# Performance work log

Hardware: AMD Instinct MI355X
Metric: run time of the kernel (lower is better)

## Reference

```python
import jax, jax.numpy as jnp
import numpy as np

HEADS = 8; KVH = 4; HD = 64; MULT = 2; DIFF = 1; DIM = 512; K = 3
LAMBDA_INIT = 0.2          # 0.8 - 0.6*exp(-0.3*layer_idx), layer_idx=0, affine=False
EPS = 1e-8
ROPE_CONST = 10000.0


def conv2d(x, w):
    # SAME padding (=1) for k=3, stride 1, zeros padding mode, no bias
    return jax.lax.conv_general_dilated(x, w, (1, 1), [(1, 1), (1, 1)],
                                        dimension_numbers=('NCHW', 'OIHW', 'NCHW'))


def rope(x):
    # x: [B, S, h, D]; rotate interleaved pairs (torch view_as_complex layout)
    D = x.shape[-1]; S = x.shape[1]
    theta = 1.0 / (ROPE_CONST ** (jnp.arange(0, D, 2, dtype=jnp.float32) / D))
    ang = jnp.arange(S, dtype=jnp.float32)[:, None] * theta[None, :]      # [S, D/2]
    cos = jnp.cos(ang)[None, :, None, :]
    sin = jnp.sin(ang)[None, :, None, :]
    xr = x.reshape(*x.shape[:-1], D // 2, 2)
    x0, x1 = xr[..., 0], xr[..., 1]
    out = jnp.stack([x0 * cos - x1 * sin, x0 * sin + x1 * cos], axis=-1)
    return out.reshape(x.shape)


def setup_inputs() -> dict:
    key = jax.random.key(0)
    ks = jax.random.split(key, 10)
    conv_std = 1.0 / np.sqrt(DIM * K * K)
    x = jax.random.normal(ks[0], (1, 2, DIM, 64, 64), jnp.float32)
    cross = jax.random.normal(ks[1], (1, 2, DIM, 32, 32), jnp.float32)
    wq = jax.random.normal(ks[2], (HEADS * HD * MULT, DIM, K, K), jnp.float32) * conv_std
    wk = jax.random.normal(ks[3], (KVH * HD * MULT, DIM, K, K), jnp.float32) * conv_std
    wv = jax.random.normal(ks[4], (KVH * HD, DIM, K, K), jnp.float32) * conv_std
    wo = jax.random.normal(ks[5], (DIM, DIM, K, K), jnp.float32) * conv_std
    # lambda params scaled to keep exp(sum over head_dim) numerically sane
    lam_q1 = jax.random.normal(ks[6], (HEADS, HD, DIFF), jnp.float32) * 0.05
    lam_q2 = jax.random.normal(ks[7], (HEADS, HD, DIFF), jnp.float32) * 0.05
    lam_k1 = jax.random.normal(ks[8], (HEADS, HD, DIFF), jnp.float32) * 0.05
    lam_k2 = jax.random.normal(ks[9], (HEADS, HD, DIFF), jnp.float32) * 0.05
    return {'x': x, 'cross': cross, 'wq': wq, 'wk': wk, 'wv': wv, 'wo': wo,
            'lam_q1': lam_q1, 'lam_q2': lam_q2, 'lam_k1': lam_k1, 'lam_k2': lam_k2}


def reference(x, cross, wq, wk, wv, wo, lam_q1, lam_q2, lam_k1, lam_k2):
    g, b, c, H, W = x.shape
    _, _, _, Hc, Wc = cross.shape
    B = g * b; Sq = H * W; Sk = Hc * Wc
    xb = x.reshape(B, c, H, W)
    cb = cross.reshape(B, c, Hc, Wc)
    # conv QKV projections
    q = conv2d(xb, wq)                     # [B, heads*HD*MULT, H, W]
    k = conv2d(cb, wk)                     # [B, KVH*HD*MULT, Hc, Wc]
    v = conv2d(cb, wv)                     # [B, KVH*HD, Hc, Wc]
    # convert: channels are head-major -> [B, S, heads, HD*mult]
    q = q.reshape(B, HEADS, HD * MULT, Sq).transpose(0, 3, 1, 2)
    k = k.reshape(B, KVH, HD * MULT, Sk).transpose(0, 3, 1, 2)
    v = v.reshape(B, KVH, HD, Sk).transpose(0, 3, 1, 2)
    # RoPE over flattened pixel positions, rotating full HD*MULT per head
    q = rope(q)
    k = rope(k)
    # grouped-query: repeat kv heads
    rep = HEADS // KVH
    k = jnp.repeat(k, rep, axis=2)         # [B, Sk, heads, HD*MULT]
    v = jnp.repeat(v, rep, axis=2)         # [B, Sk, heads, HD]
    # split into 1+DIFF score components
    qm = q.reshape(B, Sq, HEADS, MULT, HD)
    km = k.reshape(B, Sk, HEADS, MULT, HD)
    scale = 1.0 / np.sqrt(HD)
    scores = jnp.einsum('bqhmd,bkhmd->bhmqk', qm, km) * scale
    attn = jax.nn.softmax(scores, axis=-1)               # [B, h, MULT, Sq, Sk]
    # differential lambda: ((exp(sum q1*k1) - exp(sum q2*k2)) + init) * (-1)^i
    signs = (-1.0) ** jnp.arange(1, DIFF + 1, dtype=jnp.float32)   # [DIFF]
    lam = (jnp.exp(jnp.sum(lam_q1 * lam_k1, axis=-2))
           - jnp.exp(jnp.sum(lam_q2 * lam_k2, axis=-2)) + LAMBDA_INIT) * signs  # [h, DIFF]
    combined = attn[:, :, 0] + jnp.einsum('hm,bhmqk->bhqk', lam, attn[:, :, 1:])
    out = jnp.einsum('bhqk,bkhd->bqhd', combined, v)     # [B, Sq, h, HD]
    # per-head RMSNorm (affine=False) then post-attention shift
    out = out * jax.lax.rsqrt(jnp.mean(out * out, axis=-1, keepdims=True) + EPS)
    out = out * (1.0 - LAMBDA_INIT)
    # revert to image layout and output conv
    out = out.reshape(B, Sq, HEADS * HD).transpose(0, 2, 1).reshape(B, c, H, W)
    out = conv2d(out, wo)
    return out.reshape(g, b, c, H, W)
```

## Files before the change

kernel.cpp:

```cpp
#include <hip/hip_runtime.h>


typedef __attribute__((ext_vector_type(8))) short short8;
typedef __attribute__((ext_vector_type(4))) float f32x4;
typedef unsigned short us;

__device__ __forceinline__ float bf2f(us u) {
  union { unsigned int i; float f; } v; v.i = ((unsigned int)u) << 16; return v.f;
}
__device__ __forceinline__ us f2bf(float f) {
  union { float f; unsigned int i; } v; v.f = f;
  unsigned int x = v.i;
  return (us)((x + 0x7fffu + ((x >> 16) & 1u)) >> 16);
}

typedef __attribute__((address_space(3))) unsigned int as3_uint;
typedef const __attribute__((address_space(1))) unsigned int as1_uint;
__device__ __forceinline__ void gload16(const us* g, us* l) {
  __builtin_amdgcn_global_load_lds((as1_uint*)g, (as3_uint*)l, 16, 0, 0);
}
__device__ __forceinline__ unsigned int cvt_pk_bf16(float a, float b) {
  unsigned int r;
  asm("v_cvt_pk_bf16_f32 %0, %1, %2" : "=v"(r) : "v"(a), "v"(b));
  return r;
}
__device__ __forceinline__ float fast_exp2(float x) {
  float r;
  asm("v_exp_f32 %0, %1" : "=v"(r) : "v"(x));
  return r;
}

__device__ __forceinline__ void transpose_body(
    const float* __restrict__ in, us* __restrict__ outT,
    int b, int y, int ci0, int H, int W, int logW) {
  const int C = 512;
  int padW = W + 2, Ppad = (H + 2) * padW;
  __shared__ float tile[64][65];
  int nt = W * 64;
  for (int idx = threadIdx.x; idx < nt; idx += 256) {
    int ci = idx >> logW, x = idx & (W - 1);
    tile[ci][x] = in[(((size_t)b * C + ci0 + ci) * H + y) * W + x];
  }
  __syncthreads();
  int nt2 = W * 32;
  for (int idx = threadIdx.x; idx < nt2; idx += 256) {
    int px = idx >> 5, c2 = idx & 31;
    unsigned int val = (unsigned int)f2bf(tile[c2 * 2][px]) |
                       ((unsigned int)f2bf(tile[c2 * 2 + 1][px]) << 16);
    *(unsigned int*)(outT + ((size_t)b * Ppad + (size_t)(y + 1) * padW + (px + 1)) * C +
                     ci0 + c2 * 2) = val;
  }
}

__global__ __launch_bounds__(256) void prep_all(
    const float* __restrict__ x, const float* __restrict__ cross,
    const float* __restrict__ wq, const float* __restrict__ wk,
    const float* __restrict__ wv, const float* __restrict__ wo,
    const float* __restrict__ lq1, const float* __restrict__ lq2,
    const float* __restrict__ lk1, const float* __restrict__ lk2,
    us* __restrict__ xpadT, us* __restrict__ cpadT, us* __restrict__ apad,
    us* __restrict__ oq, us* __restrict__ ok, us* __restrict__ ov,
    us* __restrict__ oo, float* __restrict__ lam) {
  int bid = blockIdx.x, tid = threadIdx.x;
  if (bid < 326) {
    int g = bid * 4 + (tid >> 6);
    int t = tid & 63;
    us* base; int W, b, i;
    if (g < 520)      { base = xpadT; W = 64; b = g >= 260; i = g - b * 260; }
    else if (g < 784) { base = cpadT; W = 32; int gg = g - 520; b = gg >= 132; i = gg - b * 132; }
    else              { base = apad; W = 64; int gg = g - 784; b = gg >= 260; i = gg - b * 260; }
    int padW = W + 2, nb = 2 * padW;
    int yy, xx;
    if (i < padW)    { yy = 0; xx = i; }
    else if (i < nb) { yy = W + 1; xx = i - padW; }
    else             { int j = i - nb; yy = 1 + (j >> 1); xx = (j & 1) * (W + 1); }
    size_t p = ((size_t)b * padW * padW + (size_t)yy * padW + xx) * 512 + t * 8;
    *(int4*)(base + p) = make_int4(0, 0, 0, 0);
  } else if (bid < 1350) {
    int i = bid - 326;
    transpose_body(x, xpadT, i >> 9, (i >> 3) & 63, (i & 7) * 64, 64, 64, 6);
  } else if (bid < 1862) {
    int i = bid - 1350;
    transpose_body(cross, cpadT, i >> 8, (i >> 3) & 31, (i & 7) * 64, 32, 32, 5);
  } else if (bid < 4166) {
    int blk = bid - 1862;
    const float* src; us* dst; int Cout, co;
    if (blk < 1024)      { src = wq; dst = oq; Cout = 1024; co = blk; }
    else if (blk < 1536) { src = wk; dst = ok; Cout = 512;  co = blk - 1024; }
    else if (blk < 1792) { src = wv; dst = ov; Cout = 256;  co = blk - 1536; }
    else                 { src = wo; dst = oo; Cout = 512;  co = blk - 1792; }
    __shared__ us l[4608];
    const float* s0 = src + (size_t)co * 4608;
#pragma unroll
    for (int k = 0; k < 18; ++k) { int i = k * 256 + tid; l[i] = f2bf(s0[i]); }
    __syncthreads();
#pragma unroll
    for (int k = 0; k < 9; ++k) {
      int j = k * 256 + tid;
      int t = j >> 8, c2 = j & 255;
      unsigned int val = (unsigned int)l[(c2 * 2) * 9 + t] |
                         ((unsigned int)l[(c2 * 2 + 1) * 9 + t] << 16);
      *(unsigned int*)(dst + (size_t)t * Cout * 512 + (size_t)co * 512 + c2 * 2) = val;
    }
  } else {
    int h = tid >> 5, d = tid & 31;
    float s1 = lq1[h * 64 + d] * lk1[h * 64 + d] +
               lq1[h * 64 + d + 32] * lk1[h * 64 + d + 32];
    float s2 = lq2[h * 64 + d] * lk2[h * 64 + d] +
               lq2[h * 64 + d + 32] * lk2[h * 64 + d + 32];
    for (int m = 16; m; m >>= 1) {
      s1 += __shfl_xor(s1, m);
      s2 += __shfl_xor(s2, m);
    }
    if (d == 0) lam[h] = -(expf(s1) - expf(s2) + 0.2f);
  }
}

__device__ __forceinline__ void conv128_body(
    const us* __restrict__ inT, const us* __restrict__ wp,
    us* __restrict__ out, int Cout, int bid, us* sh) {
  int v = (bid & 7) * 64 + (bid >> 3);
  int pxt = v & 31, cot = (v >> 5) & 7, b = v >> 8;
  int p0 = pxt * 128, co0 = cot * 128;
  int tid = threadIdx.x;
  int wave = tid >> 6, lane = tid & 63, l15 = lane & 15, hi4 = lane >> 4;
  int wr = wave >> 1, wc = wave & 1;
  f32x4 acc[4][4];
#pragma unroll
  for (int m = 0; m < 4; ++m)
#pragma unroll
    for (int n = 0; n < 4; ++n) acc[m][n] = (f32x4){0.f, 0.f, 0.f, 0.f};

  int arow[4], brow[4];
#pragma unroll
  for (int c = 0; c < 4; ++c) {
    int row = c * 32 + (tid >> 3);
    int g = (tid & 7) ^ (row & 7);
    int px = p0 + row;
    int y = px >> 6, x = px & 63;
    arow[c] = (y * 66 + x) * 512 + g * 8;
    brow[c] = (co0 + row) * 512 + g * 8;
  }
  int aoff[4][2], boff[4][2];
#pragma unroll
  for (int m = 0; m < 4; ++m)
#pragma unroll
    for (int ks = 0; ks < 2; ++ks) {
      int ra = wr * 64 + m * 16 + l15;
      int rb = wc * 64 + m * 16 + l15;
      aoff[m][ks] = ra * 64 + (((ks * 4 + hi4) ^ (l15 & 7)) * 8);
      boff[m][ks] = rb * 64 + (((ks * 4 + hi4) ^ (l15 & 7)) * 8);
    }
  const us* abase = inT + (size_t)b * 66 * 66 * 512;

  auto stage = [&](int buf, int s) {
    int tn = s >> 3, ci = (s & 7) << 6;
    int ky = (tn * 11) >> 5, kx = tn - ky * 3;
    const us* as = abase + (ky * 66 + kx) * 512 + ci;
    const us* bs = wp + (size_t)tn * Cout * 512 + ci;
    us* la = sh + buf * 16384;
    us* lb = la + 8192;
#pragma unroll
    for (int c = 0; c < 4; ++c) {
      gload16(as + arow[c], la + c * 2048 + wave * 512);
      gload16(bs + brow[c], lb + c * 2048 + wave * 512);
    }
  };

  stage(0, 0);
  __syncthreads();
  for (int s = 0; s < 72; ++s) {
    int cur = s & 1;
    if (s < 71) stage(cur ^ 1, s + 1);
    const us* la = sh + cur * 16384;
    const us* lb = la + 8192;
#pragma unroll
    for (int ks = 0; ks < 2; ++ks) {
      short8 af[4], bf[4];
#pragma unroll
      for (int m = 0; m < 4; ++m) af[m] = *(const short8*)(la + aoff[m][ks]);
#pragma unroll
      for (int n = 0; n < 4; ++n) bf[n] = *(const short8*)(lb + boff[n][ks]);
#pragma unroll
      for (int m = 0; m < 4; ++m)
#pragma unroll
        for (int n = 0; n < 4; ++n)
          acc[m][n] = __builtin_amdgcn_mfma_f32_16x16x32_bf16(af[m], bf[n], acc[m][n], 0, 0, 0);
    }
    __syncthreads();
  }
  int par = lane & 1;
#pragma unroll
  for (int n = 0; n < 4; ++n) {
    int co = co0 + wc * 64 + n * 16 + l15;
    int j = (co & 127) >> 1;
    float th = exp2f(-(float)j * 0.20762050593f);
    float sth, cth;
    sincosf(th, &sth, &cth);
#pragma unroll
    for (int m = 0; m < 4; ++m) {
      int pxb = p0 + wr * 64 + m * 16 + hi4 * 4;
      float s0, c0;
      sincosf((float)pxb * th, &s0, &c0);
#pragma unroll
      for (int r = 0; r < 4; ++r) {
        float xv = acc[m][n][r];
        float ov = __shfl_xor(xv, 1);
        float y = par ? fmaf(ov, s0, xv * c0) : fmaf(xv, c0, -ov * s0);
        out[((size_t)b * 4096 + (pxb + r)) * Cout + co] = f2bf(y);
        float c1 = c0 * cth - s0 * sth;
        s0 = fmaf(c0, sth, s0 * cth);
        c0 = c1;
      }
    }
  }
}

template <int TRANS_OUT, int ROPE>
__device__ __forceinline__ void conv64_body(
    const us* __restrict__ inT, const us* __restrict__ wp,
    us* __restrict__ out, int Cout, int logCoT, int bid, int ngrid, us* sh) {
  int nchunk = ngrid >> 3;
  int v = (bid & 7) * nchunk + (bid >> 3);
  int yt = v & 15;
  int cot = (v >> 4) & ((1 << logCoT) - 1);
  int b = v >> (4 + logCoT);
  int p0 = yt * 64, co0 = cot * 64;
  const int W = 32, logW = 5, padW = 34, HW = 1024;
  int tid = threadIdx.x;
  int wave = tid >> 6, lane = tid & 63, l15 = lane & 15, hi4 = lane >> 4;
  f32x4 acc[4];
#pragma unroll
  for (int i = 0; i < 4; ++i) acc[i] = (f32x4){0.f, 0.f, 0.f, 0.f};

  int arow[2], brow[2];
#pragma unroll
  for (int c = 0; c < 2; ++c) {
    int row = (wave * 2 + c) * 8 + (lane >> 3);
    int g = (lane & 7) ^ (row & 7);
    int px = p0 + row;
    int y = px >> logW, x = px & (W - 1);
    arow[c] = (y * padW + x) * 512 + g * 8;
    brow[c] = (co0 + row) * 512 + g * 8;
  }
  int gb[2];
#pragma unroll
  for (int ks = 0; ks < 2; ++ks) gb[ks] = ((ks * 4 + hi4) ^ (l15 & 7)) * 8;

  const us* abase = inT + (size_t)b * padW * padW * 512;

  auto stage = [&](int buf, int s) {
    int tn = s >> 3, ci = (s & 7) << 6;
    int ky = (tn * 11) >> 5, kx = tn - ky * 3;
    const us* as = abase + (ky * padW + kx) * 512 + ci;
    const us* bs = wp + (size_t)tn * Cout * 512 + ci;
    us* la = sh + buf * 8192;
    us* lb = la + 4096;
#pragma unroll
    for (int c = 0; c < 2; ++c) {
      gload16(as + arow[c], la + (wave * 2 + c) * 512);
      gload16(bs + brow[c], lb + (wave * 2 + c) * 512);
    }
  };

  stage(0, 0);
  __syncthreads();
  for (int s = 0; s < 72; ++s) {
    int cur = s & 1;
    if (s < 71) stage(cur ^ 1, s + 1);
    const us* la = sh + cur * 8192;
    const us* lb = la + 4096;
#pragma unroll
    for (int ks = 0; ks < 2; ++ks) {
      short8 bf = *(const short8*)(lb + (16 * wave + l15) * 64 + gb[ks]);
#pragma unroll
      for (int i = 0; i < 4; ++i) {
        short8 af = *(const short8*)(la + (i * 16 + l15) * 64 + gb[ks]);
        acc[i] = __builtin_amdgcn_mfma_f32_16x16x32_bf16(af, bf, acc[i], 0, 0, 0);
      }
    }
    __syncthreads();
  }
  if (ROPE) {
    int co = co0 + 16 * wave + l15;
    int j = (co & 127) >> 1;
    float th = exp2f(-(float)j * 0.20762050593f);
    float sth, cth;
    sincosf(th, &sth, &cth);
    int par = lane & 1;
#pragma unroll
    for (int i = 0; i < 4; ++i) {
      int pxb = p0 + i * 16 + hi4 * 4;
      float s0, c0;
      sincosf((float)pxb * th, &s0, &c0);
#pragma unroll
      for (int r = 0; r < 4; ++r) {
        float xv = acc[i][r];
        float ov = __shfl_xor(xv, 1);
        float y = par ? fmaf(ov, s0, xv * c0) : fmaf(xv, c0, -ov * s0);
        out[((size_t)b * HW + (pxb + r)) * Cout + co] = f2bf(y);
        float c1 = c0 * cth - s0 * sth;
        s0 = fmaf(c0, sth, s0 * cth);
        c0 = c1;
      }
    }
  } else {
#pragma unroll
    for (int i = 0; i < 4; ++i)
#pragma unroll
      for (int r = 0; r < 4; ++r) {
        int px = TRANS_OUT ? (p0 + (hi4 * 4 + r) * 4 + i)
                           : (p0 + i * 16 + hi4 * 4 + r);
        int co = co0 + 16 * wave + l15;
        us val = f2bf(acc[i][r]);
        if (TRANS_OUT)
          out[((size_t)b * Cout + co) * HW + px] = val;
        else
          out[((size_t)b * HW + px) * Cout + co] = val;
      }
  }
}

__global__ __launch_bounds__(256) void conv_qkv(
    const us* __restrict__ xpadT, const us* __restrict__ cpadT,
    const us* __restrict__ wqp, const us* __restrict__ wkp,
    const us* __restrict__ wvp, us* __restrict__ qb,
    us* __restrict__ kb, us* __restrict__ vT) {
  __shared__ __align__(16) us sh[2][2][128][64];
  int bid = blockIdx.x;
  if (bid < 256)      conv64_body<0, 1>(cpadT, wkp, kb, 512, 3, bid, 256, &sh[0][0][0][0]);
  else if (bid < 384) conv64_body<1, 0>(cpadT, wvp, vT, 256, 2, bid - 256, 128, &sh[0][0][0][0]);
  else                conv128_body(xpadT, wqp, qb, 1024, bid - 384, &sh[0][0][0][0]);
}

__global__ __launch_bounds__(256) void conv128_out(
    const us* __restrict__ apad, const us* __restrict__ wp,
    float* __restrict__ out) {
  int bid = blockIdx.x;
  int v = (bid & 7) * 32 + (bid >> 3);
  int pxt = v & 31, cot = (v >> 5) & 3, b = v >> 7;
  int p0 = pxt * 128, co0 = cot * 128;
  int tid = threadIdx.x;
  int wave = tid >> 6, lane = tid & 63, l15 = lane & 15, hi4 = lane >> 4;
  int wr = wave >> 1, wc = wave & 1;
  __shared__ __align__(16) us lds[2][2][128][64];
  f32x4 acc[4][4];
#pragma unroll
  for (int m = 0; m < 4; ++m)
#pragma unroll
    for (int n = 0; n < 4; ++n) acc[m][n] = (f32x4){0.f, 0.f, 0.f, 0.f};

  int arow[4], brow[4];
#pragma unroll
  for (int c = 0; c < 4; ++c) {
    int row = c * 32 + (tid >> 3);
    int g = (tid & 7) ^ (row & 7);
    arow[c] = (co0 + row) * 512 + g * 8;
    int px = p0 + row;
    int y = px >> 6, x = px & 63;
    brow[c] = (y * 66 + x) * 512 + g * 8;
  }
  int aoff[4][2], boff[4][2];
#pragma unroll
  for (int m = 0; m < 4; ++m)
#pragma unroll
    for (int ks = 0; ks < 2; ++ks) {
      int ra = wr * 64 + m * 16 + l15;
      int rb = wc * 64 + m * 16 + l15;
      aoff[m][ks] = ra * 64 + (((ks * 4 + hi4) ^ (l15 & 7)) * 8);
      boff[m][ks] = rb * 64 + (((ks * 4 + hi4) ^ (l15 & 7)) * 8);
    }
  const us* bbase = apad + (size_t)b * 4356 * 512;

  auto stage = [&](int buf, int s) {
    int tn = s >> 3, ci = (s & 7) << 6;
    int ky = (tn * 11) >> 5, kx = tn - ky * 3;
    const us* as = wp + (size_t)tn * 512 * 512 + ci;
    const us* bs = bbase + (ky * 66 + kx) * 512 + ci;
    us* la = &lds[buf][0][0][0];
    us* lb = &lds[buf][1][0][0];
#pragma unroll
    for (int c = 0; c < 4; ++c) {
      gload16(as + arow[c], la + c * 2048 + wave * 512);
      gload16(bs + brow[c], lb + c * 2048 + wave * 512);
    }
  };

  stage(0, 0);
  __syncthreads();
  for (int s = 0; s < 72; ++s) {
    int cur = s & 1;
    if (s < 71) stage(cur ^ 1, s + 1);
    const us* la = &lds[cur][0][0][0];
    const us* lb = &lds[cur][1][0][0];
#pragma unroll
    for (int ks = 0; ks < 2; ++ks) {
      short8 af[4], bf[4];
#pragma unroll
      for (int m = 0; m < 4; ++m) af[m] = *(const short8*)(la + aoff[m][ks]);
#pragma unroll
      for (int n = 0; n < 4; ++n) bf[n] = *(const short8*)(lb + boff[n][ks]);
#pragma unroll
      for (int m = 0; m < 4; ++m)
#pragma unroll
        for (int n = 0; n < 4; ++n)
          acc[m][n] = __builtin_amdgcn_mfma_f32_16x16x32_bf16(af[m], bf[n], acc[m][n], 0, 0, 0);
    }
    __syncthreads();
  }
#pragma unroll
  for (int m = 0; m < 4; ++m)
#pragma unroll
    for (int n = 0; n < 4; ++n)
#pragma unroll
      for (int r = 0; r < 4; ++r) {
        int co = co0 + wr * 64 + m * 16 + hi4 * 4 + r;
        int px = p0 + wc * 64 + n * 16 + l15;
        out[((size_t)b * 512 + co) * 4096 + px] = acc[m][n][r];
      }
}

__global__ __launch_bounds__(256) void attn_kernel(
    const us* __restrict__ qb, const us* __restrict__ kb,
    const us* __restrict__ vT, const float* __restrict__ lam,
    us* __restrict__ apad) {
  int qt = blockIdx.x, h = blockIdx.y, b = blockIdx.z;
  int kvh = h >> 1;
  int tid = threadIdx.x;
  int wave = tid >> 6, lane = tid & 63, l15 = lane & 15, hi4 = lane >> 4;
  __shared__ __align__(16) us Klds[2][8192];
  __shared__ __align__(16) us Vlds[2][4096];
  __shared__ __align__(16) us Plds[4][16][72];

  int q0 = qt * 128;
  short8 qf[2][2][2];
  {
    const us* qsrc =
        qb + ((size_t)(b * 4096 + q0 + wave * 32 + l15)) * 1024 + h * 128 + hi4 * 8;
#pragma unroll
    for (int mf = 0; mf < 2; ++mf)
#pragma unroll
      for (int m = 0; m < 2; ++m)
#pragma unroll
        for (int ks = 0; ks < 2; ++ks)
          qf[mf][m][ks] = *(const short8*)(qsrc + mf * 16384 + m * 64 + ks * 32);
  }

  float sumd[2][2][4];
  f32x4 accO[2][2][4];
#pragma unroll
  for (int mf = 0; mf < 2; ++mf)
#pragma unroll
    for (int m = 0; m < 2; ++m)
#pragma unroll
      for (int r = 0; r < 4; ++r) {
        sumd[mf][m][r] = 0.f;
        accO[mf][m][r] = (f32x4){0.f, 0.f, 0.f, 0.f};
      }
  float lamh = lam[h];

  const us* kbase0 = kb + (size_t)b * 524288 + kvh * 128;
  const us* vbase0 = vT + ((size_t)(b * 256 + kvh * 64)) * 1024;
  int krow[4], vrow[2];
#pragma unroll
  for (int c = 0; c < 4; ++c) {
    int row = (wave * 4 + c) * 4 + hi4;
    int g = (l15 & 8) | ((l15 & 7) ^ (row & 7));
    krow[c] = row * 512 + g * 8;
  }
#pragma unroll
  for (int c = 0; c < 2; ++c) {
    int row = (wave * 2 + c) * 8 + (lane >> 3);
    int g = (lane & 7) ^ (row & 7);
    vrow[c] = row * 1024 + g * 8;
  }
  int kg0[2], kg1[2], vg[2];
#pragma unroll
  for (int m = 0; m < 2; ++m) {
    kg0[m] = (m * 8 | (hi4 ^ (l15 & 7))) * 8;
    kg1[m] = (m * 8 | ((4 + hi4) ^ (l15 & 7))) * 8;
  }
#pragma unroll
  for (int ks = 0; ks < 2; ++ks) vg[ks] = ((ks * 4 + hi4) ^ (l15 & 7)) * 8;

  auto stage = [&](int buf, int kt2) {
    const us* kk = kbase0 + (size_t)kt2 * 32768;
    const us* vv = vbase0 + kt2 * 64;
#pragma unroll
    for (int c = 0; c < 4; ++c)
      gload16(kk + krow[c], &Klds[buf][(wave * 4 + c) * 512]);
#pragma unroll
    for (int c = 0; c < 2; ++c)
      gload16(vv + vrow[c], &Vlds[buf][(wave * 2 + c) * 512]);
  };

  const float cexp = 0.18033688f;
  stage(0, 0);
  for (int kt = 0; kt < 16; ++kt) {
    int cur = kt & 1;
    if (kt < 15) {
      stage(cur ^ 1, kt + 1);
      asm volatile("s_waitcnt vmcnt(6)" ::: "memory");
    } else {
      asm volatile("s_waitcnt vmcnt(0)" ::: "memory");
    }
    __builtin_amdgcn_s_barrier();
    __builtin_amdgcn_sched_barrier(0);

    short8 vf[2][4];
#pragma unroll
    for (int ks = 0; ks < 2; ++ks)
#pragma unroll
      for (int nf = 0; nf < 4; ++nf)
        vf[ks][nf] = *(const short8*)&Vlds[cur][(nf * 16 + l15) * 64 + vg[ks]];

#pragma unroll
    for (int m = 0; m < 2; ++m) {
      short8 kf[4][2];
#pragma unroll
      for (int nf = 0; nf < 4; ++nf) {
        kf[nf][0] = *(const short8*)&Klds[cur][(nf * 16 + l15) * 128 + kg0[m]];
        kf[nf][1] = *(const short8*)&Klds[cur][(nf * 16 + l15) * 128 + kg1[m]];
      }
#pragma unroll
      for (int mf = 0; mf < 2; ++mf) {
        f32x4 s[4];
        __builtin_amdgcn_s_setprio(1);
#pragma unroll
        for (int nf = 0; nf < 4; ++nf) {
          f32x4 z = (f32x4){0.f, 0.f, 0.f, 0.f};
          z = __builtin_amdgcn_mfma_f32_16x16x32_bf16(qf[mf][m][0], kf[nf][0], z, 0, 0, 0);
          z = __builtin_amdgcn_mfma_f32_16x16x32_bf16(qf[mf][m][1], kf[nf][1], z, 0, 0, 0);
          s[nf] = z;
        }
        __builtin_amdgcn_s_setprio(0);
#pragma unroll
        for (int r = 0; r < 4; ++r) {
          float p0 = fast_exp2(s[0][r] * cexp);
          float p1 = fast_exp2(s[1][r] * cexp);
          float p2 = fast_exp2(s[2][r] * cexp);
          float p3 = fast_exp2(s[3][r] * cexp);
          sumd[mf][m][r] += (p0 + p1) + (p2 + p3);
          unsigned int w0 = cvt_pk_bf16(p0, p1);
          unsigned int w1 = cvt_pk_bf16(p2, p3);
          *(uint2*)&Plds[wave][hi4 * 4 + r][l15 * 4] = make_uint2(w0, w1);
        }
        __builtin_amdgcn_s_setprio(1);
#pragma unroll
        for (int ks = 0; ks < 2; ++ks) {
          short8 pf = *(const short8*)&Plds[wave][l15][ks * 32 + hi4 * 8];
#pragma unroll
          for (int nf = 0; nf < 4; ++nf)
            accO[mf][m][nf] =
                __builtin_amdgcn_mfma_f32_16x16x32_bf16(pf, vf[ks][nf], accO[mf][m][nf], 0, 0, 0);
        }
        __builtin_amdgcn_s_setprio(0);
      }
    }
    asm volatile("s_waitcnt lgkmcnt(0)" ::: "memory");
    __builtin_amdgcn_s_barrier();
    __builtin_amdgcn_sched_barrier(0);
  }

#pragma unroll
  for (int mf = 0; mf < 2; ++mf)
#pragma unroll
    for (int m = 0; m < 2; ++m)
#pragma unroll
      for (int r = 0; r < 4; ++r) {
        float sx = sumd[mf][m][r];
        sx += __shfl_xor(sx, 1);
        sx += __shfl_xor(sx, 2);
        sx += __shfl_xor(sx, 4);
        sx += __shfl_xor(sx, 8);
        sumd[mf][m][r] = sx;
      }
#pragma unroll
  for (int mf = 0; mf < 2; ++mf)
#pragma unroll
    for (int r = 0; r < 4; ++r) {
      float inv0 = 1.f / sumd[mf][0][r];
      float inv1 = lamh / sumd[mf][1][r];
      float comb[4];
      float ss = 0.f;
#pragma unroll
      for (int nf = 0; nf < 4; ++nf) {
        comb[nf] = accO[mf][0][nf][r] * inv0 + accO[mf][1][nf][r] * inv1;
        ss += comb[nf] * comb[nf];
      }
      ss += __shfl_xor(ss, 1);
      ss += __shfl_xor(ss, 2);
      ss += __shfl_xor(ss, 4);
      ss += __shfl_xor(ss, 8);
      float sc = rsqrtf(ss * (1.f / 64.f) + 1e-8f) * 0.8f;
      int q = q0 + wave * 32 + mf * 16 + hi4 * 4 + r;
      int y = q >> 6, x = q & 63;
      size_t oaddr = ((size_t)b * 4356 + (size_t)(y + 1) * 66 + (x + 1)) * 512 + h * 64;
#pragma unroll
      for (int nf = 0; nf < 4; ++nf) apad[oaddr + nf * 16 + l15] = f2bf(comb[nf] * sc);
    }
}

extern "C" void kernel_launch(void* const* d_in, const int* in_sizes, int n_in,
                              void* d_out, int out_size, void* d_ws, size_t ws_size,
                              hipStream_t stream) {
  const float* x     = (const float*)d_in[0];
  const float* cross = (const float*)d_in[1];
  const float* wq    = (const float*)d_in[2];
  const float* wk    = (const float*)d_in[3];
  const float* wv    = (const float*)d_in[4];
  const float* wo    = (const float*)d_in[5];
  const float* lq1   = (const float*)d_in[6];
  const float* lq2   = (const float*)d_in[7];
  const float* lk1   = (const float*)d_in[8];
  const float* lk2   = (const float*)d_in[9];
  float* out = (float*)d_out;

  char* ws = (char*)d_ws;
  size_t off = 0;
  auto nxt = [&](size_t bytes) { char* p = ws + off; off += bytes; return p; };
  us* xpadT = (us*)nxt(8921088);
  us* cpadT = (us*)nxt(2367488);
  us* apad  = (us*)nxt(8921088);
  us* wqp = (us*)nxt(9437184);
  us* wkp = (us*)nxt(4718592);
  us* wvp = (us*)nxt(2359296);
  us* wop = (us*)nxt(4718592);
  us* qb  = (us*)nxt(16777216);
  us* kb  = (us*)nxt(2097152);
  us* vT  = (us*)nxt(1048576);
  float* lam = (float*)nxt(256);
  (void)ws_size; (void)in_sizes; (void)n_in; (void)out_size;

  prep_all<<<4167, 256, 0, stream>>>(x, cross, wq, wk, wv, wo,
                                     lq1, lq2, lk1, lk2,
                                     xpadT, cpadT, apad, wqp, wkp, wvp, wop, lam);
  conv_qkv<<<896, 256, 0, stream>>>(xpadT, cpadT, wqp, wkp, wvp, qb, kb, vT);
  attn_kernel<<<dim3(32, 8, 2), 256, 0, stream>>>(qb, kb, vT, lam, apad);
  conv128_out<<<256, 256, 0, stream>>>(apad, wop, out);
}
```

Before: 261.2 us.

## Reuse padded input rows in LDS across 3x3 taps in Q and output convs

The Q projection conv and output conv are rewritten as one templated kernel. It stages a block of padded image rows (a halo) for a 32-channel slice into LDS once and reuses it for all nine filter taps, instead of reloading the shifted activation tile for every tap. Weights stream through a 4-deep ring buffer with explicit vmcnt waits and raw barriers. The K/V convs are split into their own launch, and the output conv now uses 128x64 tiles with twice as many blocks. This adds a kernel launch, uses finer-grained 32-channel K steps, and relies on hand-tuned wait counts whose correctness is fragile.

```diff
diff --git a/kernel.cpp b/kernel.cpp
--- a/kernel.cpp
+++ b/kernel.cpp
@@ -116,103 +116,152 @@
   }
 }
 
-__device__ __forceinline__ void conv128_body(
-    const us* __restrict__ inT, const us* __restrict__ wp,
-    us* __restrict__ out, int Cout, int bid, us* sh) {
+template <int MODE>
+__global__ __launch_bounds__(256) void conv_main(
+    const us* __restrict__ pix,
+    const us* __restrict__ wp,
+    us* __restrict__ outb, float* __restrict__ outf) {
+  constexpr int NR = (MODE == 0) ? 4 : 2;
+  constexpr int Cout = (MODE == 0) ? 1024 : 512;
+  constexpr int RROWS = (MODE == 0) ? 264 : 198;
+  constexpr int AROUNDS = (MODE == 0) ? 5 : 4;
+  int bid = blockIdx.x;
   int v = (bid & 7) * 64 + (bid >> 3);
-  int pxt = v & 31, cot = (v >> 5) & 7, b = v >> 8;
-  int p0 = pxt * 128, co0 = cot * 128;
+  int b, p0, co0;
+  if (MODE == 0) { p0 = ((v >> 3) & 31) * 128; co0 = (v & 7) * 128; b = v >> 8; }
+  else           { p0 = (v & 63) * 64; co0 = ((v >> 6) & 3) * 128; b = v >> 8; }
   int tid = threadIdx.x;
   int wave = tid >> 6, lane = tid & 63, l15 = lane & 15, hi4 = lane >> 4;
   int wr = wave >> 1, wc = wave & 1;
-  f32x4 acc[4][4];
+
+  __shared__ __align__(16) us Dbuf[4][128 * 32];
+  __shared__ __align__(16) us Res[(MODE == 0 ? 320 : 256) * 32];
+
+  f32x4 acc[4][NR];
 #pragma unroll
   for (int m = 0; m < 4; ++m)
 #pragma unroll
-    for (int n = 0; n < 4; ++n) acc[m][n] = (f32x4){0.f, 0.f, 0.f, 0.f};
-
-  int arow[4], brow[4];
-#pragma unroll
-  for (int c = 0; c < 4; ++c) {
-    int row = c * 32 + (tid >> 3);
-    int g = (tid & 7) ^ (row & 7);
-    int px = p0 + row;
-    int y = px >> 6, x = px & 63;
-    arow[c] = (y * 66 + x) * 512 + g * 8;
-    brow[c] = (co0 + row) * 512 + g * 8;
-  }
-  int aoff[4][2], boff[4][2];
-#pragma unroll
-  for (int m = 0; m < 4; ++m)
-#pragma unroll
-    for (int ks = 0; ks < 2; ++ks) {
-      int ra = wr * 64 + m * 16 + l15;
-      int rb = wc * 64 + m * 16 + l15;
-      aoff[m][ks] = ra * 64 + (((ks * 4 + hi4) ^ (l15 & 7)) * 8);
-      boff[m][ks] = rb * 64 + (((ks * 4 + hi4) ^ (l15 & 7)) * 8);
-    }
-  const us* abase = inT + (size_t)b * 66 * 66 * 512;
-
-  auto stage = [&](int buf, int s) {
-    int tn = s >> 3, ci = (s & 7) << 6;
-    int ky = (tn * 11) >> 5, kx = tn - ky * 3;
-    const us* as = abase + (ky * 66 + kx) * 512 + ci;
-    const us* bs = wp + (size_t)tn * Cout * 512 + ci;
-    us* la = sh + buf * 16384;
-    us* lb = la + 8192;
-#pragma unroll
-    for (int c = 0; c < 4; ++c) {
-      gload16(as + arow[c], la + c * 2048 + wave * 512);
-      gload16(bs + brow[c], lb + c * 2048 + wave * 512);
+    for (int n = 0; n < NR; ++n) acc[m][n] = (f32x4){0.f, 0.f, 0.f, 0.f};
+
+  int y0 = p0 >> 6;
+  const us* resg = pix + ((size_t)b * 4356 + (size_t)y0 * 66) * 512;
+  int srow = wave * 16 + (lane >> 2);
+  int sg = lane & 3;
+
+  auto stageRes = [&](int c) {
+#pragma unroll
+    for (int ar = 0; ar < AROUNDS; ++ar) {
+      int row = ar * 64 + srow;
+      int rowc = row < RROWS ? row : RROWS - 1;
+      gload16(resg + (size_t)rowc * 512 + c * 32 + ((sg ^ (rowc & 3)) * 8),
+              &Res[(ar * 64 + wave * 16) * 32]);
     }
   };
-
-  stage(0, 0);
-  __syncthreads();
-  for (int s = 0; s < 72; ++s) {
-    int cur = s & 1;
-    if (s < 71) stage(cur ^ 1, s + 1);
-    const us* la = sh + cur * 16384;
-    const us* lb = la + 8192;
-#pragma unroll
-    for (int ks = 0; ks < 2; ++ks) {
-      short8 af[4], bf[4];
-#pragma unroll
-      for (int m = 0; m < 4; ++m) af[m] = *(const short8*)(la + aoff[m][ks]);
-#pragma unroll
-      for (int n = 0; n < 4; ++n) bf[n] = *(const short8*)(lb + boff[n][ks]);
+  auto stageD = [&](int buf, int t, int c) {
+#pragma unroll
+    for (int dr = 0; dr < 2; ++dr) {
+      int row = dr * 64 + srow;
+      gload16(wp + ((size_t)t * Cout + co0 + row) * 512 + c * 32 + ((sg ^ (row & 3)) * 8),
+              &Dbuf[buf][(dr * 64 + wave * 16) * 32]);
+    }
+  };
+
+  stageRes(0);
+  stageD(0, 0, 0);
+  stageD(1, 1, 0);
+
+  for (int c = 0; c < 16; ++c) {
+#pragma unroll
+    for (int t = 0; t < 9; ++t) {
+      int s = c * 9 + t;
+      int sn = s + 2;
+      if (sn < 144) stageD((c + t + 2) & 3, sn % 9, sn / 9);
+      if (s == 143)
+        asm volatile("s_waitcnt vmcnt(0)" ::: "memory");
+      else if (s == 142 || (t == 0 && s))
+        asm volatile("s_waitcnt vmcnt(2)" ::: "memory");
+      else
+        asm volatile("s_waitcnt vmcnt(4)" ::: "memory");
+      __builtin_amdgcn_s_barrier();
+      __builtin_amdgcn_sched_barrier(0);
+
+      int ky = (t * 11) >> 5, kx = t - ky * 3;
+      const us* db = &Dbuf[(c + t) & 3][0];
+      short8 af[4], bf[NR];
+      if (MODE == 0) {
+#pragma unroll
+        for (int m = 0; m < 4; ++m) {
+          int row = (wr + ky) * 66 + m * 16 + l15 + kx;
+          af[m] = *(const short8*)&Res[row * 32 + ((hi4 ^ (row & 3)) * 8)];
+        }
+#pragma unroll
+        for (int n = 0; n < NR; ++n) {
+          int row = wc * 64 + n * 16 + l15;
+          bf[n] = *(const short8*)(db + row * 32 + ((hi4 ^ (row & 3)) * 8));
+        }
+      } else {
+#pragma unroll
+        for (int m = 0; m < 4; ++m) {
+          int row = wr * 64 + m * 16 + l15;
+          af[m] = *(const short8*)(db + row * 32 + ((hi4 ^ (row & 3)) * 8));
+        }
+#pragma unroll
+        for (int n = 0; n < NR; ++n) {
+          int row = ky * 66 + wc * 32 + n * 16 + l15 + kx;
+          bf[n] = *(const short8*)&Res[row * 32 + ((hi4 ^ (row & 3)) * 8)];
+        }
+      }
 #pragma unroll
       for (int m = 0; m < 4; ++m)
 #pragma unroll
-        for (int n = 0; n < 4; ++n)
+        for (int n = 0; n < NR; ++n)
           acc[m][n] = __builtin_amdgcn_mfma_f32_16x16x32_bf16(af[m], bf[n], acc[m][n], 0, 0, 0);
-    }
-    __syncthreads();
-  }
-  int par = lane & 1;
-#pragma unroll
-  for (int n = 0; n < 4; ++n) {
-    int co = co0 + wc * 64 + n * 16 + l15;
-    int j = (co & 127) >> 1;
-    float th = exp2f(-(float)j * 0.20762050593f);
-    float sth, cth;
-    sincosf(th, &sth, &cth);
-#pragma unroll
-    for (int m = 0; m < 4; ++m) {
-      int pxb = p0 + wr * 64 + m * 16 + hi4 * 4;
-      float s0, c0;
-      sincosf((float)pxb * th, &s0, &c0);
-#pragma unroll
-      for (int r = 0; r < 4; ++r) {
-        float xv = acc[m][n][r];
-        float ov = __shfl_xor(xv, 1);
-        float y = par ? fmaf(ov, s0, xv * c0) : fmaf(xv, c0, -ov * s0);
-        out[((size_t)b * 4096 + (pxb + r)) * Cout + co] = f2bf(y);
-        float c1 = c0 * cth - s0 * sth;
-        s0 = fmaf(c0, sth, s0 * cth);
-        c0 = c1;
-      }
-    }
+
+      if (t == 8 && c < 15) {
+        __builtin_amdgcn_s_barrier();
+        __builtin_amdgcn_sched_barrier(0);
+        stageRes(c + 1);
+      }
+    }
+  }
+
+  if (MODE == 0) {
+    int par = lane & 1;
+#pragma unroll
+    for (int n = 0; n < NR; ++n) {
+      int co = co0 + wc * 64 + n * 16 + l15;
+      int j = (co & 127) >> 1;
+      float th = exp2f(-(float)j * 0.20762050593f);
+      float sth, cth;
+      sincosf(th, &sth, &cth);
+#pragma unroll
+      for (int m = 0; m < 4; ++m) {
+        int pxb = p0 + wr * 64 + m * 16 + hi4 * 4;
+        float s0, c0;
+        sincosf((float)pxb * th, &s0, &c0);
+#pragma unroll
+        for (int r = 0; r < 4; ++r) {
+          float xv = acc[m][n][r];
+          float ov = __shfl_xor(xv, 1);
+          float y = par ? fmaf(ov, s0, xv * c0) : fmaf(xv, c0, -ov * s0);
+          outb[((size_t)b * 4096 + (pxb + r)) * 1024 + co] = f2bf(y);
+          float c1 = c0 * cth - s0 * sth;
+          s0 = fmaf(c0, sth, s0 * cth);
+          c0 = c1;
+        }
+      }
+    }
+  } else {
+#pragma unroll
+    for (int m = 0; m < 4; ++m)
+#pragma unroll
+      for (int n = 0; n < NR; ++n)
+#pragma unroll
+        for (int r = 0; r < 4; ++r) {
+          int co = co0 + wr * 64 + m * 16 + hi4 * 4 + r;
+          int px = p0 + wc * 32 + n * 16 + l15;
+          outf[((size_t)b * 512 + co) * 4096 + px] = acc[m][n][r];
+        }
   }
 }
 
@@ -321,103 +370,13 @@
   }
 }
 
-__global__ __launch_bounds__(256) void conv_qkv(
-    const us* __restrict__ xpadT, const us* __restrict__ cpadT,
-    const us* __restrict__ wqp, const us* __restrict__ wkp,
-    const us* __restrict__ wvp, us* __restrict__ qb,
-    us* __restrict__ kb, us* __restrict__ vT) {
-  __shared__ __align__(16) us sh[2][2][128][64];
+__global__ __launch_bounds__(256) void conv64_all(
+    const us* __restrict__ cpadT, const us* __restrict__ wkp,
+    const us* __restrict__ wvp, us* __restrict__ kb, us* __restrict__ vT) {
+  __shared__ __align__(16) us sh[2][2][64][64];
   int bid = blockIdx.x;
-  if (bid < 256)      conv64_body<0, 1>(cpadT, wkp, kb, 512, 3, bid, 256, &sh[0][0][0][0]);
-  else if (bid < 384) conv64_body<1, 0>(cpadT, wvp, vT, 256, 2, bid - 256, 128, &sh[0][0][0][0]);
-  else                conv128_body(xpadT, wqp, qb, 1024, bid - 384, &sh[0][0][0][0]);
-}
-
-__global__ __launch_bounds__(256) void conv128_out(
-    const us* __restrict__ apad, const us* __restrict__ wp,
-    float* __restrict__ out) {
-  int bid = blockIdx.x;
-  int v = (bid & 7) * 32 + (bid >> 3);
-  int pxt = v & 31, cot = (v >> 5) & 3, b = v >> 7;
-  int p0 = pxt * 128, co0 = cot * 128;
-  int tid = threadIdx.x;
-  int wave = tid >> 6, lane = tid & 63, l15 = lane & 15, hi4 = lane >> 4;
-  int wr = wave >> 1, wc = wave & 1;
-  __shared__ __align__(16) us lds[2][2][128][64];
-  f32x4 acc[4][4];
-#pragma unroll
-  for (int m = 0; m < 4; ++m)
-#pragma unroll
-    for (int n = 0; n < 4; ++n) acc[m][n] = (f32x4){0.f, 0.f, 0.f, 0.f};
-
-  int arow[4], brow[4];
-#pragma unroll
-  for (int c = 0; c < 4; ++c) {
-    int row = c * 32 + (tid >> 3);
-    int g = (tid & 7) ^ (row & 7);
-    arow[c] = (co0 + row) * 512 + g * 8;
-    int px = p0 + row;
-    int y = px >> 6, x = px & 63;
-    brow[c] = (y * 66 + x) * 512 + g * 8;
-  }
-  int aoff[4][2], boff[4][2];
-#pragma unroll
-  for (int m = 0; m < 4; ++m)
-#pragma unroll
-    for (int ks = 0; ks < 2; ++ks) {
-      int ra = wr * 64 + m * 16 + l15;
-      int rb = wc * 64 + m * 16 + l15;
-      aoff[m][ks] = ra * 64 + (((ks * 4 + hi4) ^ (l15 & 7)) * 8);
-      boff[m][ks] = rb * 64 + (((ks * 4 + hi4) ^ (l15 & 7)) * 8);
-    }
-  const us* bbase = apad + (size_t)b * 4356 * 512;
-
-  auto stage = [&](int buf, int s) {
-    int tn = s >> 3, ci = (s & 7) << 6;
-    int ky = (tn * 11) >> 5, kx = tn - ky * 3;
-    const us* as = wp + (size_t)tn * 512 * 512 + ci;
-    const us* bs = bbase + (ky * 66 + kx) * 512 + ci;
-    us* la = &lds[buf][0][0][0];
-    us* lb = &lds[buf][1][0][0];
-#pragma unroll
-    for (int c = 0; c < 4; ++c) {
-      gload16(as + arow[c], la + c * 2048 + wave * 512);
-      gload16(bs + brow[c], lb + c * 2048 + wave * 512);
-    }
-  };
-
-  stage(0, 0);
-  __syncthreads();
-  for (int s = 0; s < 72; ++s) {
-    int cur = s & 1;
-    if (s < 71) stage(cur ^ 1, s + 1);
-    const us* la = &lds[cur][0][0][0];
-    const us* lb = &lds[cur][1][0][0];
-#pragma unroll
-    for (int ks = 0; ks < 2; ++ks) {
-      short8 af[4], bf[4];
-#pragma unroll
-      for (int m = 0; m < 4; ++m) af[m] = *(const short8*)(la + aoff[m][ks]);
-#pragma unroll
-      for (int n = 0; n < 4; ++n) bf[n] = *(const short8*)(lb + boff[n][ks]);
-#pragma unroll
-      for (int m = 0; m < 4; ++m)
-#pragma unroll
-        for (int n = 0; n < 4; ++n)
-          acc[m][n] = __builtin_amdgcn_mfma_f32_16x16x32_bf16(af[m], bf[n], acc[m][n], 0, 0, 0);
-    }
-    __syncthreads();
-  }
-#pragma unroll
-  for (int m = 0; m < 4; ++m)
-#pragma unroll
-    for (int n = 0; n < 4; ++n)
-#pragma unroll
-      for (int r = 0; r < 4; ++r) {
-        int co = co0 + wr * 64 + m * 16 + hi4 * 4 + r;
-        int px = p0 + wc * 64 + n * 16 + l15;
-        out[((size_t)b * 512 + co) * 4096 + px] = acc[m][n][r];
-      }
+  if (bid < 256) conv64_body<0, 1>(cpadT, wkp, kb, 512, 3, bid, 256, &sh[0][0][0][0]);
+  else           conv64_body<1, 0>(cpadT, wvp, vT, 256, 2, bid - 256, 128, &sh[0][0][0][0]);
 }
 
 __global__ __launch_bounds__(256) void attn_kernel(
@@ -635,7 +594,8 @@
   prep_all<<<4167, 256, 0, stream>>>(x, cross, wq, wk, wv, wo,
                                      lq1, lq2, lk1, lk2,
                                      xpadT, cpadT, apad, wqp, wkp, wvp, wop, lam);
-  conv_qkv<<<896, 256, 0, stream>>>(xpadT, cpadT, wqp, wkp, wvp, qb, kb, vT);
+  conv64_all<<<384, 256, 0, stream>>>(cpadT, wkp, wvp, kb, vT);
+  conv_main<0><<<512, 256, 0, stream>>>(xpadT, wqp, qb, nullptr);
   attn_kernel<<<dim3(32, 8, 2), 256, 0, stream>>>(qb, kb, vT, lam, apad);
-  conv128_out<<<256, 256, 0, stream>>>(apad, wop, out);
-}
+  conv_main<1><<<512, 256, 0, stream>>>(apad, wop, nullptr, out);
+}
```

Result: slower. 270.2 us (+3.4%).
